# Optimization experiments

Measured on AMD Instinct MI355X. Metric: run time of the kernel, lower is better.

The kernel has to match this reference:

```python
import jax, jax.numpy as jnp
import numpy as np

K = 8          # knn neighbors
NS = 12        # nscale
NG = 6         # nscale // 2
NBLOCK = 3
TAU = 10.0
SLOPE = 0.2    # LeakyReLU negative slope
HEADS = 2      # att
B, N = 2, 4096


def _lrelu(x):
    return jax.nn.leaky_relu(x, SLOPE)


def _knn_idx(x, k):
    # x: [B,N,F] -> idx of k nearest neighbors (self excluded): [B,N,k]
    d2 = jnp.sum(x * x, axis=-1)                      # [B,N]
    dist = d2[:, :, None] + d2[:, None, :] - 2.0 * jnp.einsum('bnf,bmf->bnm', x, x)
    n = x.shape[1]
    dist = dist + jnp.eye(n, dtype=x.dtype) * 1e9     # exclude self loops
    _, idx = jax.lax.top_k(-dist, k)
    return idx


def _gat_conv(x, idx, W, a_src, a_dst):
    # x: [B,N,F], idx: [B,N,K], W: [F,H,D], a_src/a_dst: [H,D]
    h = jnp.einsum('bnf,fhd->bnhd', x, W)             # [B,N,H,D]
    hj = jax.vmap(lambda hb, ib: hb[ib])(h, idx)      # gather neighbors [B,N,K,H,D]
    e = _lrelu(jnp.einsum('bnhd,hd->bnh', h, a_src)[:, :, None, :]
               + jnp.einsum('bnkhd,hd->bnkh', hj, a_dst))
    alpha = jax.nn.softmax(e, axis=2)                 # softmax over K neighbors
    # aggregate and average over heads
    return jnp.einsum('bnkh,bnkhd->bnd', alpha, hj) / HEADS


def _fe(x, idx, m, P):
    # FeatureExtraction: 2 GAT convs with LeakyReLU between them
    h = _lrelu(_gat_conv(x, idx, P['W1'][m], P['a1s'][m], P['a1d'][m]))
    return _gat_conv(h, idx, P['W2'][m], P['a2s'][m], P['a2d'][m])


def _gumbel_hard(logits, g):
    # F.gumbel_softmax(..., tau=TAU, hard=True, dim=2) with pre-drawn gumbel noise g
    y = jax.nn.softmax((logits + g) / TAU, axis=2)
    hard = jax.nn.one_hot(jnp.argmax(y, axis=2), logits.shape[2], dtype=y.dtype)
    return hard + y - jax.lax.stop_gradient(y)  # straight-through


def _forward(d1, gumbel, W1, a1s, a1d, W2, a2s, a2d):
    P = dict(W1=W1, a1s=a1s, a1d=a1d, W2=W2, a2s=a2s, a2d=a2d)
    b, n = d1.shape[0], d1.shape[1]
    d1_xy = d1[:, :, 0:2]
    xs = []
    for i in range(NBLOCK):
        idx = _knn_idx(d1, K)
        feats = _lrelu(_fe(d1[:, :, 2:], idx, 2 * i, P))      # [B,N,12]
        w1 = _fe(feats, idx, 2 * i + 1, P)                    # [B,N,12]
        oh1 = _gumbel_hard(w1[:, :, 0::2], gumbel[i, 0])
        x1 = jnp.sum(d1[:, :, 2::2] * oh1, axis=2, keepdims=True)   # [B,N,1]
        oh2 = _gumbel_hard(w1[:, :, 1::2], gumbel[i, 1])
        x2 = jnp.sum(d1[:, :, 3::2] * oh2, axis=2, keepdims=True)
        xs.append(jnp.concatenate([x1, x2], axis=2))
        if i == NBLOCK - 1:
            break
        # x1_expand: channel 0 interleaves x1 (even) / x2 (odd), channel 1 = d1 feats
        ch0 = jnp.stack([jnp.broadcast_to(x1, (b, n, NG)),
                         jnp.broadcast_to(x2, (b, n, NG))], axis=-1).reshape(b, n, NS)
        x1_expand = jnp.stack([ch0, d1[:, :, 2:]], axis=-1)   # [B,N,12,2]
        dxa = jnp.abs(d1[:, :, 2::2] - x1)
        dxb = jnp.abs(d1[:, :, 3::2] - x2)
        x1f_in = jnp.stack([dxa, dxb], axis=-1).reshape(b, n, NS)  # interleaved
        xf = _lrelu(_fe(x1f_in, idx, 6 + 3 * i, P))
        x_ws = _fe(xf, idx, 6 + 3 * i + 1, P)
        d_ws = _fe(feats, idx, 6 + 3 * i + 2, P)
        wbar = jax.nn.softmax(jnp.stack([x_ws, d_ws], axis=-1), axis=-1)  # [B,N,12,2]
        d12 = jnp.sum(wbar * x1_expand, axis=-1)
        d1 = jnp.concatenate([d1_xy, d12], axis=2)
    return jnp.stack(xs)  # [NBLOCK, B, N, 2]


def setup_inputs() -> dict:
    key = jax.random.key(0)
    ks = jax.random.split(key, 9)
    d1 = jax.random.normal(ks[0], (B, N, 2 + NS), dtype=jnp.float32)
    u = jax.random.uniform(ks[1], (NBLOCK, 2, B, N, NG), dtype=jnp.float32,
                           minval=1e-6, maxval=1.0 - 1e-6)
    gumbel = -jnp.log(-jnp.log(u))
    M = 12  # 6 attention + 6 expand FeatureExtraction modules, identical shapes
    s = 0.1
    return {
        'd1': d1,
        'gumbel': gumbel,
        'W1': jax.random.normal(ks[2], (M, NS, HEADS, 32), dtype=jnp.float32) * s,
        'a1_src': jax.random.normal(ks[3], (M, HEADS, 32), dtype=jnp.float32) * s,
        'a1_dst': jax.random.normal(ks[4], (M, HEADS, 32), dtype=jnp.float32) * s,
        'W2': jax.random.normal(ks[5], (M, 32, HEADS, NS), dtype=jnp.float32) * s,
        'a2_src': jax.random.normal(ks[6], (M, HEADS, NS), dtype=jnp.float32) * s,
        'a2_dst': jax.random.normal(ks[7], (M, HEADS, NS), dtype=jnp.float32) * s,
    }


def reference(d1, gumbel, W1, a1_src, a1_dst, W2, a2_src, a2_dst):
    return _forward(d1, gumbel, W1, a1_src, a1_dst, W2, a2_src, a2_dst)
```

## Files before the change

kernel.cpp:

```cpp
#include <hip/hip_runtime.h>
#include <float.h>

#define K_NN 8
#define NS 12
#define NG 6
#define NBLOCK 3
#define HEADS 2
#define BB 2
#define NPTS 4096
#define NN (BB*NPTS)
#define NF 14
#define XPS 16

__device__ __forceinline__ float lrelu(float x) { return x >= 0.f ? x : 0.2f * x; }

__global__ __launch_bounds__(256) void prep_kernel(const float* __restrict__ d1_in,
                                                   float* __restrict__ d1c,
                                                   float* __restrict__ Xp) {
  const int n = blockIdx.x * 256 + threadIdx.x;
  if (n >= NN) return;
  float v[NF];
#pragma unroll
  for (int f = 0; f < NF; ++f) v[f] = d1_in[(size_t)n * NF + f];
#pragma unroll
  for (int f = 0; f < NF; ++f) d1c[(size_t)n * NF + f] = v[f];
  float s = 0.f;
#pragma unroll
  for (int f = 0; f < NF; ++f) s += v[f] * v[f];
#pragma unroll
  for (int f = 0; f < NF; ++f) Xp[(size_t)n * XPS + f] = v[f];
  Xp[(size_t)n * XPS + 14] = s;
  Xp[(size_t)n * XPS + 15] = 0.f;
}

__global__ __launch_bounds__(256) void knn_kernel(const float* __restrict__ Xp,
                                                  int* __restrict__ idxo) {
  const int wave = threadIdx.x >> 6;
  const int lane = threadIdx.x & 63;
  const int r = blockIdx.x * 4 + wave;
  const int b = r >> 12;
  const int rl = r & (NPTS - 1);
  const float* __restrict__ Xb = Xp + (size_t)b * NPTS * XPS;

  float xr[NF];
#pragma unroll
  for (int f = 0; f < NF; ++f) xr[f] = Xb[(size_t)rl * XPS + f];
  const float d2n = Xb[(size_t)rl * XPS + 14];

  unsigned long long kb[8];
#pragma unroll
  for (int p = 0; p < 8; ++p) kb[p] = ~0ull;

  const float* pc = Xb + (size_t)lane * XPS;
  float4 c0 = *(const float4*)(pc);
  float4 c1 = *(const float4*)(pc + 4);
  float4 c2 = *(const float4*)(pc + 8);
  float4 c3 = *(const float4*)(pc + 12);

  for (int t = 0; t < NPTS / 64; ++t) {
    const int tn = (t + 1 < NPTS / 64) ? (t + 1) : 0;
    const float* pn = Xb + (size_t)(tn * 64 + lane) * XPS;
    const float4 n0 = *(const float4*)(pn);
    const float4 n1 = *(const float4*)(pn + 4);
    const float4 n2 = *(const float4*)(pn + 8);
    const float4 n3 = *(const float4*)(pn + 12);

    const int m = t * 64 + lane;
    float dot = 0.f;
    dot += xr[0] * c0.x;  dot += xr[1] * c0.y;
    dot += xr[2] * c0.z;  dot += xr[3] * c0.w;
    dot += xr[4] * c1.x;  dot += xr[5] * c1.y;
    dot += xr[6] * c1.z;  dot += xr[7] * c1.w;
    dot += xr[8] * c2.x;  dot += xr[9] * c2.y;
    dot += xr[10] * c2.z; dot += xr[11] * c2.w;
    dot += xr[12] * c3.x; dot += xr[13] * c3.y;
    const float dist = d2n + c3.z - 2.0f * dot;

    unsigned long long key =
        ((unsigned long long)__float_as_uint(dist) << 32) | (unsigned)m;
    if (m == rl) key = ~0ull;

    while (__any(key < kb[7])) {
      unsigned long long v = key;
#pragma unroll
      for (int off = 32; off > 0; off >>= 1) {
        const unsigned long long ov = __shfl_xor(v, off);
        if (ov < v) v = ov;
      }
      unsigned long long cv = v;
#pragma unroll
      for (int p = 0; p < 8; ++p) {
        if (cv < kb[p]) { const unsigned long long tv = kb[p]; kb[p] = cv; cv = tv; }
      }
      if (key == v) key = ~0ull;
    }

    c0 = n0; c1 = n1; c2 = n2; c3 = n3;
  }

  if (lane == 0) {
    const size_t ob = (size_t)r * K_NN;
#pragma unroll
    for (int p = 0; p < 8; ++p)
      idxo[ob + p] = b * NPTS + (int)(kb[p] & 0xFFFFFFFFull);
  }
}

template <int F, int DH>
__global__ __launch_bounds__(256) void proj_kernel(const float* __restrict__ x, int ldx,
                                                   const float* __restrict__ W,
                                                   const float* __restrict__ asrc,
                                                   const float* __restrict__ adst,
                                                   float* __restrict__ hout,
                                                   float* __restrict__ sdout) {
  constexpr int TWO_DH = 2 * DH;
  __shared__ float Wl[F * TWO_DH];
  __shared__ float asl[TWO_DH];
  __shared__ float adl[TWO_DH];
  for (int i = threadIdx.x; i < F * TWO_DH; i += 256) Wl[i] = W[i];
  for (int i = threadIdx.x; i < TWO_DH; i += 256) { asl[i] = asrc[i]; adl[i] = adst[i]; }
  __syncthreads();

  const int gid = blockIdx.x * 256 + threadIdx.x;
  const int n = gid >> 1;
  const int hh = gid & 1;
  if (n >= NN) return;

  float xv[F];
#pragma unroll
  for (int f = 0; f < F; ++f) xv[f] = x[(size_t)n * ldx + f];

  const int o0 = hh * DH;
  float h[DH];
#pragma unroll
  for (int j = 0; j < DH; ++j) {
    float acc = 0.f;
#pragma unroll
    for (int f = 0; f < F; ++f) acc += xv[f] * Wl[f * TWO_DH + o0 + j];
    h[j] = acc;
  }
  float sp = 0.f, tp = 0.f;
#pragma unroll
  for (int j = 0; j < DH; ++j) { sp += h[j] * asl[o0 + j]; tp += h[j] * adl[o0 + j]; }

#pragma unroll
  for (int j = 0; j < DH; ++j) hout[(size_t)n * TWO_DH + o0 + j] = h[j];

  const float so = __shfl_xor(sp, 1);
  const float to = __shfl_xor(tp, 1);
  if (hh == 0) {
    float4 sd = make_float4(sp, so, tp, to);
    *(float4*)&sdout[(size_t)n * 4] = sd;
  }
}

template <int DH, int DS, bool LR>
__global__ __launch_bounds__(256) void agg_kernel(const float* __restrict__ h,
                                                  const float* __restrict__ sd,
                                                  const int* __restrict__ idx,
                                                  float* __restrict__ yout) {
  constexpr int PER = DH / DS;
  const int gid = blockIdx.x * 256 + threadIdx.x;
  const int n = gid / DS;
  const int dc = gid % DS;
  if (n >= NN) return;

  const float4 s4 = *(const float4*)&sd[(size_t)n * 4];
  const float s0 = s4.x, s1 = s4.y;

  int jj[K_NN];
#pragma unroll
  for (int k = 0; k < K_NN; ++k) jj[k] = idx[(size_t)n * K_NN + k];

  float e0[K_NN], e1[K_NN];
#pragma unroll
  for (int k = 0; k < K_NN; ++k) {
    const float4 t4 = *(const float4*)&sd[(size_t)jj[k] * 4];
    e0[k] = lrelu(s0 + t4.z);
    e1[k] = lrelu(s1 + t4.w);
  }
  float m0 = -FLT_MAX, m1 = -FLT_MAX;
#pragma unroll
  for (int k = 0; k < K_NN; ++k) { m0 = fmaxf(m0, e0[k]); m1 = fmaxf(m1, e1[k]); }
  float w0[K_NN], w1[K_NN], S0 = 0.f, S1 = 0.f;
#pragma unroll
  for (int k = 0; k < K_NN; ++k) {
    w0[k] = __expf(e0[k] - m0); S0 += w0[k];
    w1[k] = __expf(e1[k] - m1); S1 += w1[k];
  }
  const float r0 = 0.5f / S0, r1 = 0.5f / S1;

  const int d0 = dc * PER;
  float y[PER];
#pragma unroll
  for (int d = 0; d < PER; ++d) y[d] = 0.f;
#pragma unroll
  for (int k = 0; k < K_NN; ++k) {
    const float* hj = h + (size_t)jj[k] * 2 * DH + d0;
    const float a0 = w0[k] * r0, a1 = w1[k] * r1;
#pragma unroll
    for (int d = 0; d < PER; ++d) y[d] += a0 * hj[d] + a1 * hj[DH + d];
  }
#pragma unroll
  for (int d = 0; d < PER; ++d) yout[(size_t)n * DH + d0 + d] = LR ? lrelu(y[d]) : y[d];
}

__global__ __launch_bounds__(256) void sel_kernel(const float* __restrict__ d1c,
                                                  const float* __restrict__ w1o,
                                                  const float* __restrict__ gum,
                                                  int blk, float* __restrict__ out,
                                                  float* __restrict__ x12,
                                                  float* __restrict__ x1f, int writeX1f) {
  const int n = blockIdx.x * 256 + threadIdx.x;
  if (n >= NN) return;
  const int b = n >> 12, nl = n & (NPTS - 1);
  const float* g1 = gum + (((size_t)(blk * 2 + 0) * BB + b) * NPTS + nl) * NG;
  const float* g2 = gum + (((size_t)(blk * 2 + 1) * BB + b) * NPTS + nl) * NG;
  const float* w = w1o + (size_t)n * NS;
  const float* dr = d1c + (size_t)n * NF;

  float best1 = -FLT_MAX, best2 = -FLT_MAX;
  int a1 = 0, a2 = 0;
#pragma unroll
  for (int a = 0; a < NG; ++a) {
    float l1 = w[2 * a] + g1[a];
    if (l1 > best1) { best1 = l1; a1 = a; }
    float l2 = w[2 * a + 1] + g2[a];
    if (l2 > best2) { best2 = l2; a2 = a; }
  }
  const float x1 = dr[2 + 2 * a1];
  const float x2 = dr[3 + 2 * a2];

  const size_t ob = (((size_t)blk * BB + b) * NPTS + nl) * 2;
  out[ob + 0] = x1;
  out[ob + 1] = x2;
  x12[n * 2 + 0] = x1;
  x12[n * 2 + 1] = x2;

  if (writeX1f) {
#pragma unroll
    for (int g = 0; g < NG; ++g) {
      x1f[(size_t)n * NS + 2 * g]     = fabsf(dr[2 + 2 * g] - x1);
      x1f[(size_t)n * NS + 2 * g + 1] = fabsf(dr[3 + 2 * g] - x2);
    }
  }
}

__global__ __launch_bounds__(256) void combine_kernel(float* __restrict__ d1c,
                                                      const float* __restrict__ xws,
                                                      const float* __restrict__ dws,
                                                      const float* __restrict__ x12,
                                                      float* __restrict__ Xp) {
  const int n = blockIdx.x * 256 + threadIdx.x;
  if (n >= NN) return;
  const float x1 = x12[n * 2 + 0], x2 = x12[n * 2 + 1];
  float* dr = d1c + (size_t)n * NF;
  const float xy0 = dr[0], xy1 = dr[1];
  float nd[NS];
#pragma unroll
  for (int c = 0; c < NS; ++c) {
    const float a = xws[(size_t)n * NS + c];
    const float dd = dws[(size_t)n * NS + c];
    const float m = fmaxf(a, dd);
    const float ea = __expf(a - m), ed = __expf(dd - m);
    const float inv = 1.f / (ea + ed);
    const float ch0 = (c & 1) ? x2 : x1;
    nd[c] = (ea * inv) * ch0 + (ed * inv) * dr[2 + c];
  }
#pragma unroll
  for (int c = 0; c < NS; ++c) dr[2 + c] = nd[c];
  float s = 0.f;
  s += xy0 * xy0;
  s += xy1 * xy1;
#pragma unroll
  for (int c = 0; c < NS; ++c) s += nd[c] * nd[c];
#pragma unroll
  for (int c = 0; c < NS; ++c) Xp[(size_t)n * XPS + 2 + c] = nd[c];
  Xp[(size_t)n * XPS + 14] = s;
}

extern "C" void kernel_launch(void* const* d_in, const int* in_sizes, int n_in,
                              void* d_out, int out_size, void* d_ws, size_t ws_size,
                              hipStream_t stream) {
  const float* d1_in = (const float*)d_in[0];
  const float* gum   = (const float*)d_in[1];
  const float* W1    = (const float*)d_in[2];
  const float* a1s   = (const float*)d_in[3];
  const float* a1d   = (const float*)d_in[4];
  const float* W2    = (const float*)d_in[5];
  const float* a2s   = (const float*)d_in[6];
  const float* a2d   = (const float*)d_in[7];
  float* out = (float*)d_out;

  float* ws     = (float*)d_ws;
  float* d1c    = ws;
  int*   idxb   = (int*)(ws + 114688);
  float* spare  = ws + 114688 + 65536;
  float* hbuf   = spare + 8192;
  float* sdb    = hbuf + 524288;
  float* ybuf   = sdb + 32768;
  float* feats  = ybuf + 262144;
  float* bufw1  = feats + 98304;
  float* bufxfi = bufw1 + 98304;
  float* bufxf  = bufxfi + 98304;
  float* bufdws = bufxf + 98304;
  float* x12    = bufdws + 98304;
  float* Xp     = x12 + 16384;

  const int NB = NN / 256;

  prep_kernel<<<NB, 256, 0, stream>>>(d1_in, d1c, Xp);

  auto run_fe = [&](const float* xin, int ldx, int m, float* yout, bool lrelu_out) {
    proj_kernel<12, 32><<<NB * 2, 256, 0, stream>>>(xin, ldx, W1 + (size_t)m * 768,
                                                    a1s + (size_t)m * 64, a1d + (size_t)m * 64,
                                                    hbuf, sdb);
    agg_kernel<32, 8, true><<<NB * 8, 256, 0, stream>>>(hbuf, sdb, idxb, ybuf);
    proj_kernel<32, 12><<<NB * 2, 256, 0, stream>>>(ybuf, 32, W2 + (size_t)m * 768,
                                                    a2s + (size_t)m * 24, a2d + (size_t)m * 24,
                                                    hbuf, sdb);
    if (lrelu_out)
      agg_kernel<12, 4, true><<<NB * 4, 256, 0, stream>>>(hbuf, sdb, idxb, yout);
    else
      agg_kernel<12, 4, false><<<NB * 4, 256, 0, stream>>>(hbuf, sdb, idxb, yout);
  };

  for (int i = 0; i < NBLOCK; ++i) {
    knn_kernel<<<NN / 4, 256, 0, stream>>>(Xp, idxb);
    run_fe(d1c + 2, NF, 2 * i, feats, true);
    run_fe(feats, NS, 2 * i + 1, bufw1, false);
    sel_kernel<<<NB, 256, 0, stream>>>(d1c, bufw1, gum, i, out, x12, bufxfi,
                                       (i < NBLOCK - 1) ? 1 : 0);
    if (i == NBLOCK - 1) break;
    run_fe(bufxfi, NS, 6 + 3 * i, bufxf, true);
    run_fe(bufxf, NS, 6 + 3 * i + 1, bufw1, false);
    run_fe(feats, NS, 6 + 3 * i + 2, bufdws, false);
    combine_kernel<<<NB, 256, 0, stream>>>(d1c, bufw1, bufdws, x12, Xp);
  }
}
```

Measured before the change: 706.2 us.

## Process two query rows per wave in knn and use float-min shuffle selection

Each wavefront in the knn kernel now handles two query rows, so every candidate tile loaded from memory is reused for two distance computations, and the grid is halved. The warp-wide minimum reduction now shuffles 32-bit floats instead of 64-bit keys, and a ballot plus find-first-set recovers the winning lane's index. This roughly halves the cost of the shuffle reduction and cuts redundant candidate loads, but doubles per-thread registers for query rows and top-k buffers, which may lower occupancy. The two insertion loops still run one after the other.

```diff
diff --git a/kernel.cpp b/kernel.cpp
--- a/kernel.cpp
+++ b/kernel.cpp
@@ -37,19 +37,24 @@
                                                   int* __restrict__ idxo) {
   const int wave = threadIdx.x >> 6;
   const int lane = threadIdx.x & 63;
-  const int r = blockIdx.x * 4 + wave;
-  const int b = r >> 12;
-  const int rl = r & (NPTS - 1);
+  const int rp = blockIdx.x * 4 + wave;
+  const int r0 = rp * 2;
+  const int b = r0 >> 12;
+  const int rl0 = r0 & (NPTS - 1);
+  const int rl1 = rl0 + 1;
   const float* __restrict__ Xb = Xp + (size_t)b * NPTS * XPS;
 
-  float xr[NF];
-#pragma unroll
-  for (int f = 0; f < NF; ++f) xr[f] = Xb[(size_t)rl * XPS + f];
-  const float d2n = Xb[(size_t)rl * XPS + 14];
-
-  unsigned long long kb[8];
-#pragma unroll
-  for (int p = 0; p < 8; ++p) kb[p] = ~0ull;
+  float xr0[NF], xr1[NF];
+#pragma unroll
+  for (int f = 0; f < NF; ++f) xr0[f] = Xb[(size_t)rl0 * XPS + f];
+#pragma unroll
+  for (int f = 0; f < NF; ++f) xr1[f] = Xb[(size_t)rl1 * XPS + f];
+  const float d2n0 = Xb[(size_t)rl0 * XPS + 14];
+  const float d2n1 = Xb[(size_t)rl1 * XPS + 14];
+
+  unsigned long long kb0[8], kb1[8];
+#pragma unroll
+  for (int p = 0; p < 8; ++p) { kb0[p] = ~0ull; kb1[p] = ~0ull; }
 
   const float* pc = Xb + (size_t)lane * XPS;
   float4 c0 = *(const float4*)(pc);
@@ -66,43 +71,76 @@
     const float4 n3 = *(const float4*)(pn + 12);
 
     const int m = t * 64 + lane;
-    float dot = 0.f;
-    dot += xr[0] * c0.x;  dot += xr[1] * c0.y;
-    dot += xr[2] * c0.z;  dot += xr[3] * c0.w;
-    dot += xr[4] * c1.x;  dot += xr[5] * c1.y;
-    dot += xr[6] * c1.z;  dot += xr[7] * c1.w;
-    dot += xr[8] * c2.x;  dot += xr[9] * c2.y;
-    dot += xr[10] * c2.z; dot += xr[11] * c2.w;
-    dot += xr[12] * c3.x; dot += xr[13] * c3.y;
-    const float dist = d2n + c3.z - 2.0f * dot;
-
-    unsigned long long key =
-        ((unsigned long long)__float_as_uint(dist) << 32) | (unsigned)m;
-    if (m == rl) key = ~0ull;
-
-    while (__any(key < kb[7])) {
-      unsigned long long v = key;
-#pragma unroll
-      for (int off = 32; off > 0; off >>= 1) {
-        const unsigned long long ov = __shfl_xor(v, off);
-        if (ov < v) v = ov;
+
+    float dot0 = 0.f;
+    dot0 += xr0[0] * c0.x;  dot0 += xr0[1] * c0.y;
+    dot0 += xr0[2] * c0.z;  dot0 += xr0[3] * c0.w;
+    dot0 += xr0[4] * c1.x;  dot0 += xr0[5] * c1.y;
+    dot0 += xr0[6] * c1.z;  dot0 += xr0[7] * c1.w;
+    dot0 += xr0[8] * c2.x;  dot0 += xr0[9] * c2.y;
+    dot0 += xr0[10] * c2.z; dot0 += xr0[11] * c2.w;
+    dot0 += xr0[12] * c3.x; dot0 += xr0[13] * c3.y;
+    float d0 = d2n0 + c3.z - 2.0f * dot0;
+
+    float dot1 = 0.f;
+    dot1 += xr1[0] * c0.x;  dot1 += xr1[1] * c0.y;
+    dot1 += xr1[2] * c0.z;  dot1 += xr1[3] * c0.w;
+    dot1 += xr1[4] * c1.x;  dot1 += xr1[5] * c1.y;
+    dot1 += xr1[6] * c1.z;  dot1 += xr1[7] * c1.w;
+    dot1 += xr1[8] * c2.x;  dot1 += xr1[9] * c2.y;
+    dot1 += xr1[10] * c2.z; dot1 += xr1[11] * c2.w;
+    dot1 += xr1[12] * c3.x; dot1 += xr1[13] * c3.y;
+    float d1 = d2n1 + c3.z - 2.0f * dot1;
+
+    unsigned long long k0 =
+        ((unsigned long long)__float_as_uint(d0) << 32) | (unsigned)m;
+    unsigned long long k1 =
+        ((unsigned long long)__float_as_uint(d1) << 32) | (unsigned)m;
+    if (m == rl0) { d0 = FLT_MAX; k0 = ~0ull; }
+    if (m == rl1) { d1 = FLT_MAX; k1 = ~0ull; }
+
+    while (__any(k0 < kb0[7])) {
+      float v = d0;
+#pragma unroll
+      for (int off = 32; off > 0; off >>= 1) v = fminf(v, __shfl_xor(v, off));
+      const unsigned long long mk = __ballot(d0 == v);
+      const int src = __ffsll((unsigned long long)mk) - 1;
+      unsigned long long kv =
+          ((unsigned long long)__float_as_uint(v) << 32) | (unsigned)(t * 64 + src);
+#pragma unroll
+      for (int p = 0; p < 8; ++p) {
+        if (kv < kb0[p]) { const unsigned long long tv = kb0[p]; kb0[p] = kv; kv = tv; }
       }
-      unsigned long long cv = v;
+      if (lane == src) { d0 = FLT_MAX; k0 = ~0ull; }
+    }
+
+    while (__any(k1 < kb1[7])) {
+      float v = d1;
+#pragma unroll
+      for (int off = 32; off > 0; off >>= 1) v = fminf(v, __shfl_xor(v, off));
+      const unsigned long long mk = __ballot(d1 == v);
+      const int src = __ffsll((unsigned long long)mk) - 1;
+      unsigned long long kv =
+          ((unsigned long long)__float_as_uint(v) << 32) | (unsigned)(t * 64 + src);
 #pragma unroll
       for (int p = 0; p < 8; ++p) {
-        if (cv < kb[p]) { const unsigned long long tv = kb[p]; kb[p] = cv; cv = tv; }
+        if (kv < kb1[p]) { const unsigned long long tv = kb1[p]; kb1[p] = kv; kv = tv; }
       }
-      if (key == v) key = ~0ull;
+      if (lane == src) { d1 = FLT_MAX; k1 = ~0ull; }
     }
 
     c0 = n0; c1 = n1; c2 = n2; c3 = n3;
   }
 
   if (lane == 0) {
-    const size_t ob = (size_t)r * K_NN;
+    const size_t ob0 = (size_t)r0 * K_NN;
 #pragma unroll
     for (int p = 0; p < 8; ++p)
-      idxo[ob + p] = b * NPTS + (int)(kb[p] & 0xFFFFFFFFull);
+      idxo[ob0 + p] = b * NPTS + (int)(kb0[p] & 0xFFFFFFFFull);
+    const size_t ob1 = (size_t)(r0 + 1) * K_NN;
+#pragma unroll
+    for (int p = 0; p < 8; ++p)
+      idxo[ob1 + p] = b * NPTS + (int)(kb1[p] & 0xFFFFFFFFull);
   }
 }
 
@@ -326,7 +364,7 @@
   };
 
   for (int i = 0; i < NBLOCK; ++i) {
-    knn_kernel<<<NN / 4, 256, 0, stream>>>(Xp, idxb);
+    knn_kernel<<<NN / 8, 256, 0, stream>>>(Xp, idxb);
     run_fe(d1c + 2, NF, 2 * i, feats, true);
     run_fe(feats, NS, 2 * i + 1, bufw1, false);
     sel_kernel<<<NB, 256, 0, stream>>>(d1c, bufw1, gum, i, out, x12, bufxfi,
```

After: 637.8 us. -9.7%, faster.
